# Optimization experiments

Hardware: AMD Instinct MI355X
Metric: run time of the kernel (lower is better)

## Reference

```python
import jax, jax.numpy as jnp
import numpy as np

NUMERICAL_STABILIZER = 1e-3


def relu_kernel(data, projection_matrix):
    # data: [B,L,H,D], projection_matrix: [M,D] -> [B,L,H,M]
    ratio = 1.0 / jnp.sqrt(jnp.asarray(projection_matrix.shape[0], dtype=data.dtype))
    data_dash = ratio * jnp.einsum('blhd,md->blhm', data, projection_matrix)
    return jax.nn.relu(data_dash) + NUMERICAL_STABILIZER


def favor_causal(query, key, value, projection_matrix):
    # query/key/value: [B,L,H,D]; projection_matrix: [M,D]
    qp = relu_kernel(query, projection_matrix)  # [B,L,H,M]
    kp = relu_kernel(key, projection_matrix)    # [B,L,H,M]
    # move L to scan axis: [L,B,H,*]
    qs = jnp.transpose(qp, (1, 0, 2, 3))
    ks = jnp.transpose(kp, (1, 0, 2, 3))
    vs = jnp.transpose(value, (1, 0, 2, 3))

    B, H, M = qs.shape[1], qs.shape[2], qs.shape[3]
    D = vs.shape[3]
    kv0 = jnp.zeros((B, H, M, D), dtype=qs.dtype)
    ksum0 = jnp.zeros((B, H, M), dtype=qs.dtype)

    def step(carry, inp):
        kv_sum, k_sum = carry
        q_t, k_t, v_t = inp  # [B,H,M], [B,H,M], [B,H,D]
        kv_sum = kv_sum + jnp.einsum('bhm,bhd->bhmd', k_t, v_t)
        k_sum = k_sum + k_t
        num_t = jnp.einsum('bhmd,bhm->bhd', kv_sum, q_t)  # [B,H,D]
        den_t = jnp.einsum('bhm,bhm->bh', q_t, k_sum)     # [B,H]
        return (kv_sum, k_sum), (num_t, den_t)

    _, (num, den) = jax.lax.scan(step, (kv0, ksum0), (qs, ks, vs))
    # num: [L,B,H,D], den: [L,B,H]
    out = num / den[..., None]
    return jnp.transpose(out, (1, 0, 2, 3))  # [B,L,H,D]


def setup_inputs() -> dict:
    key = jax.random.key(0)
    k1, k2, k3, k4 = jax.random.split(key, 4)
    B, L, H, D, M = 2, 4096, 8, 64, 128
    return {
        'query': jax.random.normal(k1, (B, L, H, D), dtype=jnp.float32),
        'key': jax.random.normal(k2, (B, L, H, D), dtype=jnp.float32),
        'value': jax.random.normal(k3, (B, L, H, D), dtype=jnp.float32),
        'projection_matrix': jax.random.normal(k4, (M, D), dtype=jnp.float32),
    }


def reference(query, key, value, projection_matrix):
    return favor_causal(query, key, value, projection_matrix)
```

## Files before the change

kernel.cpp:

```cpp
#include <hip/hip_runtime.h>


#define B_ 2
#define L_ 4096
#define H_ 8
#define D_ 64
#define M_ 128
#define BH_ 16
#define HD_ 512
#define LHD_ (L_*HD_)
#define C_ 64
#define T_ 64
#define RATIO 0.08838834764831845f
#define EPS 1e-3f

#define REC_CS 8320
#define REC_F  8192
#define QF_OFF 8519680
#define N2_OFF 16908288
#define RS_OFF 25296896
#define P_OFF  25427968

#define VT_S  72
#define KFT_S 72
#define TM_S  136

typedef __attribute__((ext_vector_type(8))) short bf16x8;
typedef __attribute__((ext_vector_type(4))) short bf16x4;
typedef __attribute__((ext_vector_type(4))) float f32x4;

__device__ __forceinline__ short f2bf(float f) {
  union { float f; unsigned u; } x; x.f = f;
  unsigned r = (x.u + 0x7fffu + ((x.u >> 16) & 1u)) >> 16;
  return (short)r;
}
__device__ __forceinline__ float bf2f(short s) {
  union { unsigned u; float f; } x; x.u = ((unsigned)(unsigned short)s) << 16;
  return x.f;
}
__device__ __forceinline__ bf16x8 load_cvt8(const float* p) {
  float4 a = *(const float4*)p;
  float4 b = *(const float4*)(p + 4);
  union { bf16x8 v; short s[8]; } u;
  u.s[0]=f2bf(a.x); u.s[1]=f2bf(a.y); u.s[2]=f2bf(a.z); u.s[3]=f2bf(a.w);
  u.s[4]=f2bf(b.x); u.s[5]=f2bf(b.y); u.s[6]=f2bf(b.z); u.s[7]=f2bf(b.w);
  return u.v;
}
#define MFMA(a,b,c) __builtin_amdgcn_mfma_f32_16x16x32_bf16((a),(b),(c),0,0,0)

__global__ __launch_bounds__(256) void k0(
    const float* __restrict__ P, unsigned short* __restrict__ ws)
{
  const int i = (blockIdx.x*256 + threadIdx.x)*4;
  float4 p4 = *(const float4*)(P + i);
  union { bf16x4 v; short s[4]; } u;
  u.s[0]=f2bf(p4.x); u.s[1]=f2bf(p4.y); u.s[2]=f2bf(p4.z); u.s[3]=f2bf(p4.w);
  *(bf16x4*)(ws + P_OFF + i) = u.v;
}

__global__ __launch_bounds__(256) void k1(
    const float* __restrict__ qq, const float* __restrict__ kk,
    const float* __restrict__ vv, unsigned short* __restrict__ ws)
{
  __shared__ short Vt[64*VT_S];
  __shared__ short Kft[128*KFT_S];
  __shared__ short KfTM[64*TM_S];
  __shared__ short QfTM[64*TM_S];

  const int tid = threadIdx.x, bid = blockIdx.x;
  const int bh = bid >> 6, c = bid & 63;
  const int b = bh >> 3, h = bh & 7;
  const int lane = tid & 63, w = tid >> 6, quad = lane >> 4, l15 = lane & 15;
  const size_t gbase = (size_t)b*LHD_ + (size_t)h*D_;
  const int t0 = c*T_;
  const unsigned short* Pb = ws + P_OFF;

  for (int fi = tid; fi < 64*16; fi += 256) {
    int t = fi >> 4, d4 = (fi & 15)*4;
    float4 v4 = *(const float4*)(vv + gbase + (size_t)(t0+t)*HD_ + d4);
    Vt[(d4+0)*VT_S + t] = f2bf(v4.x);
    Vt[(d4+1)*VT_S + t] = f2bf(v4.y);
    Vt[(d4+2)*VT_S + t] = f2bf(v4.z);
    Vt[(d4+3)*VT_S + t] = f2bf(v4.w);
  }

  const float* qrow = qq + gbase + (size_t)(t0 + 16*w + l15)*HD_;
  const float* krow = kk + gbase + (size_t)(t0 + 16*w + l15)*HD_;
  bf16x8 bq0 = load_cvt8(qrow + quad*8);
  bf16x8 bq1 = load_cvt8(qrow + 32 + quad*8);
  bf16x8 bk0 = load_cvt8(krow + quad*8);
  bf16x8 bk1 = load_cvt8(krow + 32 + quad*8);
  #pragma unroll
  for (int ct = 0; ct < 8; ++ct) {
    bf16x8 ap0 = *(const bf16x8*)(Pb + (ct*16 + l15)*64 + quad*8);
    bf16x8 ap1 = *(const bf16x8*)(Pb + (ct*16 + l15)*64 + 32 + quad*8);
    f32x4 qa = {0.f,0.f,0.f,0.f}, ka = {0.f,0.f,0.f,0.f};
    qa = MFMA(ap0,bq0,qa); qa = MFMA(ap1,bq1,qa);
    ka = MFMA(ap0,bk0,ka); ka = MFMA(ap1,bk1,ka);
    union { bf16x4 v; short s[4]; } pq, pk;
    #pragma unroll
    for (int reg = 0; reg < 4; ++reg) {
      int m = 16*ct + 4*quad + reg;
      short qv = f2bf(fmaxf(qa[reg]*RATIO, 0.f) + EPS);
      short kv = f2bf(fmaxf(ka[reg]*RATIO, 0.f) + EPS);
      pq.s[reg] = qv; pk.s[reg] = kv;
      Kft[m*KFT_S + 16*w + l15] = kv;
    }
    *(bf16x4*)&QfTM[(16*w+l15)*TM_S + 16*ct + 4*quad] = pq.v;
    *(bf16x4*)&KfTM[(16*w+l15)*TM_S + 16*ct + 4*quad] = pk.v;
  }
  __syncthreads();

  unsigned short* csb = ws + (size_t)(bh*C_+c)*REC_CS;
  unsigned short* qfb = ws + QF_OFF + (size_t)(bh*C_+c)*REC_F;

  {
    int tt = tid >> 4, mb = (tid & 15)*8;
    #pragma unroll
    for (int j = 0; j < 4; ++j) {
      bf16x8 v8 = *(const bf16x8*)&QfTM[(tt + 16*j)*TM_S + mb];
      *(bf16x8*)(qfb + (tt + 16*j)*128 + mb) = v8;
    }
  }
  bf16x8 qfr[4];
  #pragma unroll
  for (int ks2 = 0; ks2 < 4; ++ks2)
    qfr[ks2] = *(const bf16x8*)&QfTM[(16*w+l15)*TM_S + ks2*32 + quad*8];

  if (tid < 128) {
    float s = 0.f;
    #pragma unroll
    for (int i = 0; i < 8; ++i) {
      bf16x8 r = *(const bf16x8*)&Kft[tid*KFT_S + 8*i];
      #pragma unroll
      for (int j = 0; j < 8; ++j) s += bf2f(r[j]);
    }
    csb[64*128 + tid] = (unsigned short)f2bf(s);
  }

  {
    bf16x8 av0 = *(const bf16x8*)&Vt[(16*w + l15)*VT_S + quad*8];
    bf16x8 av1 = *(const bf16x8*)&Vt[(16*w + l15)*VT_S + 32 + quad*8];
    #pragma unroll
    for (int mt = 0; mt < 8; ++mt) {
      bf16x8 b0 = *(const bf16x8*)&Kft[(16*mt + l15)*KFT_S + quad*8];
      bf16x8 b1 = *(const bf16x8*)&Kft[(16*mt + l15)*KFT_S + 32 + quad*8];
      f32x4 acc = {0.f,0.f,0.f,0.f};
      acc = MFMA(b0, av0, acc);
      acc = MFMA(b1, av1, acc);
      union { bf16x4 v; short s[4]; } pc;
      #pragma unroll
      for (int reg = 0; reg < 4; ++reg) pc.s[reg] = f2bf(acc[reg]);
      *(bf16x4*)(csb + (16*w + l15)*128 + 16*mt + 4*quad) = pc.v;
    }
  }
  __syncthreads();

  short* Sm = QfTM;

  f32x4 sacc[4];
  #pragma unroll
  for (int jt = 0; jt < 4; ++jt) { f32x4 z = {0.f,0.f,0.f,0.f}; sacc[jt] = z; }
  #pragma unroll
  for (int ks2 = 0; ks2 < 4; ++ks2) {
    #pragma unroll
    for (int jt = 0; jt < 4; ++jt) {
      bf16x8 bb = *(const bf16x8*)&KfTM[(16*jt + l15)*TM_S + ks2*32 + quad*8];
      sacc[jt] = MFMA(qfr[ks2], bb, sacc[jt]);
    }
  }
  float rs[4] = {0.f,0.f,0.f,0.f};
  #pragma unroll
  for (int jt = 0; jt < 4; ++jt)
    #pragma unroll
    for (int reg = 0; reg < 4; ++reg) {
      int row = 16*w + 4*quad + reg;
      int j = l15 + 16*jt;
      float val = (j <= row) ? sacc[jt][reg] : 0.f;
      rs[reg] += val;
      Sm[row*TM_S + j] = f2bf(val);
    }
  #pragma unroll
  for (int reg = 0; reg < 4; ++reg) {
    rs[reg] += __shfl_xor(rs[reg], 1);
    rs[reg] += __shfl_xor(rs[reg], 2);
    rs[reg] += __shfl_xor(rs[reg], 4);
    rs[reg] += __shfl_xor(rs[reg], 8);
  }
  float* rsg = (float*)(ws + RS_OFF);
  if (l15 < 4) {
    float v = (l15==0) ? rs[0] : (l15==1) ? rs[1] : (l15==2) ? rs[2] : rs[3];
    rsg[bh*L_ + t0 + 16*w + 4*quad + l15] = v;
  }

  float* n2 = (float*)(ws + N2_OFF);
  f32x4 nacc[4];
  #pragma unroll
  for (int ct = 0; ct < 4; ++ct) { f32x4 z = {0.f,0.f,0.f,0.f}; nacc[ct] = z; }
  #pragma unroll
  for (int kss = 0; kss < 2; ++kss) {
    bf16x8 sb = *(const bf16x8*)&Sm[(16*w + l15)*TM_S + kss*32 + quad*8];
    #pragma unroll
    for (int ct = 0; ct < 4; ++ct) {
      bf16x8 a = *(const bf16x8*)&Vt[(16*ct + l15)*VT_S + kss*32 + quad*8];
      nacc[ct] = MFMA(a, sb, nacc[ct]);
    }
  }
  const int tg = t0 + 16*w + l15;
  #pragma unroll
  for (int ct = 0; ct < 4; ++ct) {
    float4 o;
    o.x = nacc[ct][0]; o.y = nacc[ct][1]; o.z = nacc[ct][2]; o.w = nacc[ct][3];
    *(float4*)(n2 + gbase + (size_t)tg*HD_ + 16*ct + 4*quad) = o;
  }
}

__global__ __launch_bounds__(256) void k2(unsigned short* __restrict__ ws)
{
  const int gid = blockIdx.x*256 + threadIdx.x;
  const int bh = gid / REC_CS, e = gid % REC_CS;
  unsigned short* base = ws + (size_t)bh*C_*REC_CS + e;
  short v[64];
  #pragma unroll
  for (int c2 = 0; c2 < 64; ++c2) v[c2] = (short)base[(size_t)c2*REC_CS];
  float run = 0.f;
  #pragma unroll
  for (int c2 = 0; c2 < 64; ++c2) {
    base[(size_t)c2*REC_CS] = (unsigned short)f2bf(run);
    run += bf2f(v[c2]);
  }
}

__global__ __launch_bounds__(256) void k3(
    const unsigned short* __restrict__ ws, float* __restrict__ out)
{
  const int tid = threadIdx.x, bid = blockIdx.x;
  const int bh = bid >> 6, c = bid & 63;
  const int b = bh >> 3, h = bh & 7;
  const int lane = tid & 63, w = tid >> 6, quad = lane >> 4, l15 = lane & 15;
  const size_t gbase = (size_t)b*LHD_ + (size_t)h*D_;
  const int t0 = c*T_;
  const unsigned short* csb = ws + (size_t)(bh*C_+c)*REC_CS;
  const unsigned short* qfb = ws + QF_OFF + (size_t)(bh*C_+c)*REC_F;
  const float* n2 = (const float*)(ws + N2_OFF);
  const float* rsg = (const float*)(ws + RS_OFF);

  const int tg = t0 + 16*w + l15;

  float4 nv[4];
  #pragma unroll
  for (int ct = 0; ct < 4; ++ct)
    nv[ct] = *(const float4*)(n2 + gbase + (size_t)tg*HD_ + 16*ct + 4*quad);
  float rsv = rsg[bh*L_ + tg];

  bf16x8 qfB[4], ksf[4];
  #pragma unroll
  for (int ks2 = 0; ks2 < 4; ++ks2) {
    qfB[ks2] = *(const bf16x8*)(qfb + (16*w + l15)*128 + ks2*32 + quad*8);
    ksf[ks2] = *(const bf16x8*)(csb + 64*128 + ks2*32 + quad*8);
  }
  float dp = 0.f;
  #pragma unroll
  for (int ks2 = 0; ks2 < 4; ++ks2)
    #pragma unroll
    for (int j = 0; j < 8; ++j) dp += bf2f(qfB[ks2][j]) * bf2f(ksf[ks2][j]);
  dp += __shfl_xor(dp, 16);
  dp += __shfl_xor(dp, 32);
  float inv = 1.f / (dp + rsv);

  f32x4 nacc[4];
  #pragma unroll
  for (int ct = 0; ct < 4; ++ct) { f32x4 z = {0.f,0.f,0.f,0.f}; nacc[ct] = z; }
  #pragma unroll
  for (int ks2 = 0; ks2 < 4; ++ks2) {
    #pragma unroll
    for (int ct = 0; ct < 4; ++ct) {
      bf16x8 a = *(const bf16x8*)(csb + (16*ct + l15)*128 + ks2*32 + quad*8);
      nacc[ct] = MFMA(a, qfB[ks2], nacc[ct]);
    }
  }
  #pragma unroll
  for (int ct = 0; ct < 4; ++ct) {
    float4 o;
    o.x = (nacc[ct][0] + nv[ct].x) * inv;
    o.y = (nacc[ct][1] + nv[ct].y) * inv;
    o.z = (nacc[ct][2] + nv[ct].z) * inv;
    o.w = (nacc[ct][3] + nv[ct].w) * inv;
    *(float4*)(out + gbase + (size_t)tg*HD_ + 16*ct + 4*quad) = o;
  }
}

extern "C" void kernel_launch(void* const* d_in, const int* in_sizes, int n_in,
                              void* d_out, int out_size, void* d_ws, size_t ws_size,
                              hipStream_t stream) {
  const float* q = (const float*)d_in[0];
  const float* k = (const float*)d_in[1];
  const float* v = (const float*)d_in[2];
  const float* P = (const float*)d_in[3];
  float* out = (float*)d_out;
  unsigned short* ws = (unsigned short*)d_ws;

  dim3 blk(256);
  k0<<<dim3(8), blk, 0, stream>>>(P, ws);
  k1<<<dim3(BH_*C_), blk, 0, stream>>>(q, k, v, ws);
  k2<<<dim3(520), blk, 0, stream>>>(ws);
  k3<<<dim3(BH_*C_), blk, 0, stream>>>(ws, out);
}
```

Baseline: 133.0 us.

## Move intra-chunk causal attention into final kernel and swizzle shared memory

Moves the intra-chunk masked QK^T and S·V computation out of the first kernel and into the final output kernel. That kernel now reloads V, reads bf16 key features written to the workspace, and computes the diagonal-block contribution and row sums directly. This removes the fp32 intermediate numerator and row-sum round trip through global memory and shrinks the first kernel's shared memory. Padded LDS strides are replaced by an XOR swizzle to avoid bank conflicts. In exchange, V is read twice and bf16 key features are written and read back, which adds work to the output kernel.

Measured after the change: 139.0 us. 4.5% more time.

```diff
diff --git a/kernel.cpp b/kernel.cpp
--- a/kernel.cpp
+++ b/kernel.cpp
@@ -17,13 +17,10 @@
 #define REC_CS 8320
 #define REC_F  8192
 #define QF_OFF 8519680
-#define N2_OFF 16908288
-#define RS_OFF 25296896
-#define P_OFF  25427968
-
-#define VT_S  72
-#define KFT_S 72
-#define TM_S  136
+#define KF_OFF 16908288
+#define P_OFF  25296896
+
+#define SWZ(r,c) ((r)*64 + ((c) ^ (((r)&7)*8)))
 
 typedef __attribute__((ext_vector_type(8))) short bf16x8;
 typedef __attribute__((ext_vector_type(4))) short bf16x4;
@@ -38,9 +35,7 @@
   union { unsigned u; float f; } x; x.u = ((unsigned)(unsigned short)s) << 16;
   return x.f;
 }
-__device__ __forceinline__ bf16x8 load_cvt8(const float* p) {
-  float4 a = *(const float4*)p;
-  float4 b = *(const float4*)(p + 4);
+__device__ __forceinline__ bf16x8 cvt8(float4 a, float4 b) {
   union { bf16x8 v; short s[8]; } u;
   u.s[0]=f2bf(a.x); u.s[1]=f2bf(a.y); u.s[2]=f2bf(a.z); u.s[3]=f2bf(a.w);
   u.s[4]=f2bf(b.x); u.s[5]=f2bf(b.y); u.s[6]=f2bf(b.z); u.s[7]=f2bf(b.w);
@@ -58,14 +53,12 @@
   *(bf16x4*)(ws + P_OFF + i) = u.v;
 }
 
-__global__ __launch_bounds__(256) void k1(
+__global__ __launch_bounds__(256) void k1a(
     const float* __restrict__ qq, const float* __restrict__ kk,
     const float* __restrict__ vv, unsigned short* __restrict__ ws)
 {
-  __shared__ short Vt[64*VT_S];
-  __shared__ short Kft[128*KFT_S];
-  __shared__ short KfTM[64*TM_S];
-  __shared__ short QfTM[64*TM_S];
+  __shared__ short Vt[64*64];
+  __shared__ short Kft[128*64];
 
   const int tid = threadIdx.x, bid = blockIdx.x;
   const int bh = bid >> 6, c = bid & 63;
@@ -75,21 +68,33 @@
   const int t0 = c*T_;
   const unsigned short* Pb = ws + P_OFF;
 
+  const float* qrow = qq + gbase + (size_t)(t0 + 16*w + l15)*HD_;
+  const float* krow = kk + gbase + (size_t)(t0 + 16*w + l15)*HD_;
+  float4 q4a = *(const float4*)(qrow + quad*8);
+  float4 q4b = *(const float4*)(qrow + quad*8 + 4);
+  float4 q4c = *(const float4*)(qrow + 32 + quad*8);
+  float4 q4d = *(const float4*)(qrow + 32 + quad*8 + 4);
+  float4 k4a = *(const float4*)(krow + quad*8);
+  float4 k4b = *(const float4*)(krow + quad*8 + 4);
+  float4 k4c = *(const float4*)(krow + 32 + quad*8);
+  float4 k4d = *(const float4*)(krow + 32 + quad*8 + 4);
+
   for (int fi = tid; fi < 64*16; fi += 256) {
     int t = fi >> 4, d4 = (fi & 15)*4;
     float4 v4 = *(const float4*)(vv + gbase + (size_t)(t0+t)*HD_ + d4);
-    Vt[(d4+0)*VT_S + t] = f2bf(v4.x);
-    Vt[(d4+1)*VT_S + t] = f2bf(v4.y);
-    Vt[(d4+2)*VT_S + t] = f2bf(v4.z);
-    Vt[(d4+3)*VT_S + t] = f2bf(v4.w);
-  }
-
-  const float* qrow = qq + gbase + (size_t)(t0 + 16*w + l15)*HD_;
-  const float* krow = kk + gbase + (size_t)(t0 + 16*w + l15)*HD_;
-  bf16x8 bq0 = load_cvt8(qrow + quad*8);
-  bf16x8 bq1 = load_cvt8(qrow + 32 + quad*8);
-  bf16x8 bk0 = load_cvt8(krow + quad*8);
-  bf16x8 bk1 = load_cvt8(krow + 32 + quad*8);
+    Vt[SWZ(d4+0, t)] = f2bf(v4.x);
+    Vt[SWZ(d4+1, t)] = f2bf(v4.y);
+    Vt[SWZ(d4+2, t)] = f2bf(v4.z);
+    Vt[SWZ(d4+3, t)] = f2bf(v4.w);
+  }
+
+  bf16x8 bq0 = cvt8(q4a, q4b), bq1 = cvt8(q4c, q4d);
+  bf16x8 bk0 = cvt8(k4a, k4b), bk1 = cvt8(k4c, k4d);
+
+  unsigned short* qfb = ws + QF_OFF + (size_t)(bh*C_+c)*REC_F;
+  unsigned short* kfb = ws + KF_OFF + (size_t)(bh*C_+c)*REC_F;
+  const int trow = 16*w + l15;
+
   #pragma unroll
   for (int ct = 0; ct < 8; ++ct) {
     bf16x8 ap0 = *(const bf16x8*)(Pb + (ct*16 + l15)*64 + quad*8);
@@ -104,34 +109,20 @@
       short qv = f2bf(fmaxf(qa[reg]*RATIO, 0.f) + EPS);
       short kv = f2bf(fmaxf(ka[reg]*RATIO, 0.f) + EPS);
       pq.s[reg] = qv; pk.s[reg] = kv;
-      Kft[m*KFT_S + 16*w + l15] = kv;
-    }
-    *(bf16x4*)&QfTM[(16*w+l15)*TM_S + 16*ct + 4*quad] = pq.v;
-    *(bf16x4*)&KfTM[(16*w+l15)*TM_S + 16*ct + 4*quad] = pk.v;
+      Kft[SWZ(m, trow)] = kv;
+    }
+    *(bf16x4*)(qfb + trow*128 + 16*ct + 4*quad) = pq.v;
+    *(bf16x4*)(kfb + trow*128 + 16*ct + 4*quad) = pk.v;
   }
   __syncthreads();
 
   unsigned short* csb = ws + (size_t)(bh*C_+c)*REC_CS;
-  unsigned short* qfb = ws + QF_OFF + (size_t)(bh*C_+c)*REC_F;
-
-  {
-    int tt = tid >> 4, mb = (tid & 15)*8;
-    #pragma unroll
-    for (int j = 0; j < 4; ++j) {
-      bf16x8 v8 = *(const bf16x8*)&QfTM[(tt + 16*j)*TM_S + mb];
-      *(bf16x8*)(qfb + (tt + 16*j)*128 + mb) = v8;
-    }
-  }
-  bf16x8 qfr[4];
-  #pragma unroll
-  for (int ks2 = 0; ks2 < 4; ++ks2)
-    qfr[ks2] = *(const bf16x8*)&QfTM[(16*w+l15)*TM_S + ks2*32 + quad*8];
 
   if (tid < 128) {
     float s = 0.f;
     #pragma unroll
     for (int i = 0; i < 8; ++i) {
-      bf16x8 r = *(const bf16x8*)&Kft[tid*KFT_S + 8*i];
+      bf16x8 r = *(const bf16x8*)&Kft[SWZ(tid, 8*i)];
       #pragma unroll
       for (int j = 0; j < 8; ++j) s += bf2f(r[j]);
     }
@@ -139,79 +130,20 @@
   }
 
   {
-    bf16x8 av0 = *(const bf16x8*)&Vt[(16*w + l15)*VT_S + quad*8];
-    bf16x8 av1 = *(const bf16x8*)&Vt[(16*w + l15)*VT_S + 32 + quad*8];
+    bf16x8 av0 = *(const bf16x8*)&Vt[SWZ(trow, quad*8)];
+    bf16x8 av1 = *(const bf16x8*)&Vt[SWZ(trow, 32 + quad*8)];
     #pragma unroll
     for (int mt = 0; mt < 8; ++mt) {
-      bf16x8 b0 = *(const bf16x8*)&Kft[(16*mt + l15)*KFT_S + quad*8];
-      bf16x8 b1 = *(const bf16x8*)&Kft[(16*mt + l15)*KFT_S + 32 + quad*8];
+      bf16x8 b0 = *(const bf16x8*)&Kft[SWZ(16*mt + l15, quad*8)];
+      bf16x8 b1 = *(const bf16x8*)&Kft[SWZ(16*mt + l15, 32 + quad*8)];
       f32x4 acc = {0.f,0.f,0.f,0.f};
       acc = MFMA(b0, av0, acc);
       acc = MFMA(b1, av1, acc);
       union { bf16x4 v; short s[4]; } pc;
       #pragma unroll
       for (int reg = 0; reg < 4; ++reg) pc.s[reg] = f2bf(acc[reg]);
-      *(bf16x4*)(csb + (16*w + l15)*128 + 16*mt + 4*quad) = pc.v;
-    }
-  }
-  __syncthreads();
-
-  short* Sm = QfTM;
-
-  f32x4 sacc[4];
-  #pragma unroll
-  for (int jt = 0; jt < 4; ++jt) { f32x4 z = {0.f,0.f,0.f,0.f}; sacc[jt] = z; }
-  #pragma unroll
-  for (int ks2 = 0; ks2 < 4; ++ks2) {
-    #pragma unroll
-    for (int jt = 0; jt < 4; ++jt) {
-      bf16x8 bb = *(const bf16x8*)&KfTM[(16*jt + l15)*TM_S + ks2*32 + quad*8];
-      sacc[jt] = MFMA(qfr[ks2], bb, sacc[jt]);
-    }
-  }
-  float rs[4] = {0.f,0.f,0.f,0.f};
-  #pragma unroll
-  for (int jt = 0; jt < 4; ++jt)
-    #pragma unroll
-    for (int reg = 0; reg < 4; ++reg) {
-      int row = 16*w + 4*quad + reg;
-      int j = l15 + 16*jt;
-      float val = (j <= row) ? sacc[jt][reg] : 0.f;
-      rs[reg] += val;
-      Sm[row*TM_S + j] = f2bf(val);
-    }
-  #pragma unroll
-  for (int reg = 0; reg < 4; ++reg) {
-    rs[reg] += __shfl_xor(rs[reg], 1);
-    rs[reg] += __shfl_xor(rs[reg], 2);
-    rs[reg] += __shfl_xor(rs[reg], 4);
-    rs[reg] += __shfl_xor(rs[reg], 8);
-  }
-  float* rsg = (float*)(ws + RS_OFF);
-  if (l15 < 4) {
-    float v = (l15==0) ? rs[0] : (l15==1) ? rs[1] : (l15==2) ? rs[2] : rs[3];
-    rsg[bh*L_ + t0 + 16*w + 4*quad + l15] = v;
-  }
-
-  float* n2 = (float*)(ws + N2_OFF);
-  f32x4 nacc[4];
-  #pragma unroll
-  for (int ct = 0; ct < 4; ++ct) { f32x4 z = {0.f,0.f,0.f,0.f}; nacc[ct] = z; }
-  #pragma unroll
-  for (int kss = 0; kss < 2; ++kss) {
-    bf16x8 sb = *(const bf16x8*)&Sm[(16*w + l15)*TM_S + kss*32 + quad*8];
-    #pragma unroll
-    for (int ct = 0; ct < 4; ++ct) {
-      bf16x8 a = *(const bf16x8*)&Vt[(16*ct + l15)*VT_S + kss*32 + quad*8];
-      nacc[ct] = MFMA(a, sb, nacc[ct]);
-    }
-  }
-  const int tg = t0 + 16*w + l15;
-  #pragma unroll
-  for (int ct = 0; ct < 4; ++ct) {
-    float4 o;
-    o.x = nacc[ct][0]; o.y = nacc[ct][1]; o.z = nacc[ct][2]; o.w = nacc[ct][3];
-    *(float4*)(n2 + gbase + (size_t)tg*HD_ + 16*ct + 4*quad) = o;
+      *(bf16x4*)(csb + trow*128 + 16*mt + 4*quad) = pc.v;
+    }
   }
 }
 
@@ -232,8 +164,12 @@
 }
 
 __global__ __launch_bounds__(256) void k3(
-    const unsigned short* __restrict__ ws, float* __restrict__ out)
-{
+    const float* __restrict__ vv, const unsigned short* __restrict__ ws,
+    float* __restrict__ out)
+{
+  __shared__ short Vt[64*64];
+  __shared__ short Sm[64*64];
+
   const int tid = threadIdx.x, bid = blockIdx.x;
   const int bh = bid >> 6, c = bid & 63;
   const int b = bh >> 3, h = bh & 7;
@@ -242,21 +178,23 @@
   const int t0 = c*T_;
   const unsigned short* csb = ws + (size_t)(bh*C_+c)*REC_CS;
   const unsigned short* qfb = ws + QF_OFF + (size_t)(bh*C_+c)*REC_F;
-  const float* n2 = (const float*)(ws + N2_OFF);
-  const float* rsg = (const float*)(ws + RS_OFF);
-
-  const int tg = t0 + 16*w + l15;
-
-  float4 nv[4];
-  #pragma unroll
-  for (int ct = 0; ct < 4; ++ct)
-    nv[ct] = *(const float4*)(n2 + gbase + (size_t)tg*HD_ + 16*ct + 4*quad);
-  float rsv = rsg[bh*L_ + tg];
+  const unsigned short* kfb = ws + KF_OFF + (size_t)(bh*C_+c)*REC_F;
+  const int trow = 16*w + l15;
+  const int tg = t0 + trow;
+
+  for (int fi = tid; fi < 64*16; fi += 256) {
+    int t = fi >> 4, d4 = (fi & 15)*4;
+    float4 v4 = *(const float4*)(vv + gbase + (size_t)(t0+t)*HD_ + d4);
+    Vt[SWZ(d4+0, t)] = f2bf(v4.x);
+    Vt[SWZ(d4+1, t)] = f2bf(v4.y);
+    Vt[SWZ(d4+2, t)] = f2bf(v4.z);
+    Vt[SWZ(d4+3, t)] = f2bf(v4.w);
+  }
 
   bf16x8 qfB[4], ksf[4];
   #pragma unroll
   for (int ks2 = 0; ks2 < 4; ++ks2) {
-    qfB[ks2] = *(const bf16x8*)(qfb + (16*w + l15)*128 + ks2*32 + quad*8);
+    qfB[ks2] = *(const bf16x8*)(qfb + trow*128 + ks2*32 + quad*8);
     ksf[ks2] = *(const bf16x8*)(csb + 64*128 + ks2*32 + quad*8);
   }
   float dp = 0.f;
@@ -266,7 +204,54 @@
     for (int j = 0; j < 8; ++j) dp += bf2f(qfB[ks2][j]) * bf2f(ksf[ks2][j]);
   dp += __shfl_xor(dp, 16);
   dp += __shfl_xor(dp, 32);
+
+  f32x4 sacc[4];
+  #pragma unroll
+  for (int jt = 0; jt < 4; ++jt) { f32x4 z = {0.f,0.f,0.f,0.f}; sacc[jt] = z; }
+  #pragma unroll
+  for (int ks2 = 0; ks2 < 4; ++ks2) {
+    #pragma unroll
+    for (int jt = 0; jt < 4; ++jt) {
+      bf16x8 bb = *(const bf16x8*)(kfb + (16*jt + l15)*128 + ks2*32 + quad*8);
+      sacc[jt] = MFMA(qfB[ks2], bb, sacc[jt]);
+    }
+  }
+  __syncthreads();
+
+  float rs[4] = {0.f,0.f,0.f,0.f};
+  #pragma unroll
+  for (int jt = 0; jt < 4; ++jt)
+    #pragma unroll
+    for (int reg = 0; reg < 4; ++reg) {
+      int row = 16*w + 4*quad + reg;
+      int j = l15 + 16*jt;
+      float val = (j <= row) ? sacc[jt][reg] : 0.f;
+      rs[reg] += val;
+      Sm[SWZ(row, j)] = f2bf(val);
+    }
+  #pragma unroll
+  for (int reg = 0; reg < 4; ++reg) {
+    rs[reg] += __shfl_xor(rs[reg], 1);
+    rs[reg] += __shfl_xor(rs[reg], 2);
+    rs[reg] += __shfl_xor(rs[reg], 4);
+    rs[reg] += __shfl_xor(rs[reg], 8);
+  }
+  float rsv_ = (l15 < 4) ? ((l15==0)?rs[0]:(l15==1)?rs[1]:(l15==2)?rs[2]:rs[3]) : 0.f;
+  float rsv = __shfl(rsv_, ((l15 >> 2) << 4) + (l15 & 3), 64);
   float inv = 1.f / (dp + rsv);
+
+  f32x4 macc[4];
+  #pragma unroll
+  for (int ct = 0; ct < 4; ++ct) { f32x4 z = {0.f,0.f,0.f,0.f}; macc[ct] = z; }
+  #pragma unroll
+  for (int kss = 0; kss < 2; ++kss) {
+    bf16x8 sb = *(const bf16x8*)&Sm[SWZ(trow, kss*32 + quad*8)];
+    #pragma unroll
+    for (int ct = 0; ct < 4; ++ct) {
+      bf16x8 a = *(const bf16x8*)&Vt[SWZ(16*ct + l15, kss*32 + quad*8)];
+      macc[ct] = MFMA(a, sb, macc[ct]);
+    }
+  }
 
   f32x4 nacc[4];
   #pragma unroll
@@ -282,10 +267,10 @@
   #pragma unroll
   for (int ct = 0; ct < 4; ++ct) {
     float4 o;
-    o.x = (nacc[ct][0] + nv[ct].x) * inv;
-    o.y = (nacc[ct][1] + nv[ct].y) * inv;
-    o.z = (nacc[ct][2] + nv[ct].z) * inv;
-    o.w = (nacc[ct][3] + nv[ct].w) * inv;
+    o.x = (nacc[ct][0] + macc[ct][0]) * inv;
+    o.y = (nacc[ct][1] + macc[ct][1]) * inv;
+    o.z = (nacc[ct][2] + macc[ct][2]) * inv;
+    o.w = (nacc[ct][3] + macc[ct][3]) * inv;
     *(float4*)(out + gbase + (size_t)tg*HD_ + 16*ct + 4*quad) = o;
   }
 }
@@ -302,7 +287,7 @@
 
   dim3 blk(256);
   k0<<<dim3(8), blk, 0, stream>>>(P, ws);
-  k1<<<dim3(BH_*C_), blk, 0, stream>>>(q, k, v, ws);
+  k1a<<<dim3(BH_*C_), blk, 0, stream>>>(q, k, v, ws);
   k2<<<dim3(520), blk, 0, stream>>>(ws);
-  k3<<<dim3(BH_*C_), blk, 0, stream>>>(ws, out);
-}
+  k3<<<dim3(BH_*C_), blk, 0, stream>>>(v, ws, out);
+}
```
